# Performance work log

Hardware: AMD Instinct MI355X
Metric: run time of the kernel (lower is better)

## Reference

```python
import jax, jax.numpy as jnp
import numpy as np

# init_kwargs: conv_k=1, scale=1
CONV_K = 1
P = 3 - CONV_K          # scale == 1 branch
PAD_X = (P + 1) // 2    # 1 (applied before: top/left)
PAD_Y = P // 2          # 1 (applied after: bottom/right)


def setup_inputs() -> dict:
    key = jax.random.key(0)
    x = jax.random.normal(key, (16, 256, 128, 128), dtype=jnp.float32)
    return {"x": x}


def reference(x):
    # Fixed FIR kernel f = [1,3,3,1]; norm_fir_k -> 2D outer product, normalized.
    f1 = jnp.array([1.0, 3.0, 3.0, 1.0], dtype=x.dtype)
    k = jnp.outer(f1, f1)
    k = k / jnp.sum(k)
    # upfirdn2d performs true convolution (kernel flipped); symmetric here but kept for fidelity.
    k = jnp.flip(k, (0, 1))
    C = x.shape[1]
    w = jnp.broadcast_to(k[None, None], (C, 1, 4, 4))  # depthwise filter
    out = jax.lax.conv_general_dilated(
        x, w,
        window_strides=(1, 1),
        padding=((PAD_X, PAD_Y), (PAD_X, PAD_Y)),
        feature_group_count=C,
        dimension_numbers=("NCHW", "OIHW", "NCHW"),
    )
    # out: [16, 256, 127, 127] = H + padX + padY - 4 + 1
    return out
```

## Files before the change

### kernel.cpp

```cpp
#include <hip/hip_runtime.h>


#define IH 128
#define IW 128
#define OH 127
#define OW 127

__global__ __launch_bounds__(128)
void upfirdn2d_blur_kernel(const float* __restrict__ x, float* __restrict__ out) {
    const int img = blockIdx.x;
    const int tx  = threadIdx.x;

    const float* __restrict__ in = x   + (size_t)img * (IH * IW);
    float*       __restrict__ o  = out + (size_t)img * (OH * OW);

    const bool active = (tx < OW);

    const float mL = (tx >= 1)      ? 1.0f : 0.0f;
    const float mR = (tx + 2 < IW)  ? 1.0f : 0.0f;
    const int xl = (tx >= 1)      ? tx - 1 : 0;
    const int x1 = (tx + 1 < IW)  ? tx + 1 : IW - 1;
    const int xr = (tx + 2 < IW)  ? tx + 2 : IW - 1;

    auto hrow = [&](int r) -> float {
        const float* __restrict__ p = in + r * IW;
        return mL * p[xl] + 3.0f * (p[tx] + p[x1]) + mR * p[xr];
    };

    float hm1 = 0.0f;
    float h0  = hrow(0);
    float h1  = hrow(1);

    #pragma unroll 2
    for (int y = 0; y < OH - 1; ++y) {
        const float h2 = hrow(y + 2);
        if (active)
            o[y * OW + tx] = (hm1 + 3.0f * (h0 + h1) + h2) * 0.015625f;
        hm1 = h0; h0 = h1; h1 = h2;
    }
    if (active)
        o[(OH - 1) * OW + tx] = (hm1 + 3.0f * (h0 + h1)) * 0.015625f;
}

extern "C" void kernel_launch(void* const* d_in, const int* in_sizes, int n_in,
                              void* d_out, int out_size, void* d_ws, size_t ws_size,
                              hipStream_t stream) {
    const float* x = (const float*)d_in[0];
    float* out = (float*)d_out;
    const int n_imgs = 16 * 256;
    hipLaunchKernelGGL(upfirdn2d_blur_kernel, dim3(n_imgs), dim3(128), 0, stream,
                       x, out);
}
```

Baseline: 473.7 us.

## Vectorize blur with float4 row loads, wave shuffles, and row-split threads

Each thread now loads four adjacent input pixels as a float4 and gets its horizontal neighbours through wave shuffles, so the redundant overlapping scalar loads go away. Each image's 128 threads are split into four groups of 32 lanes, and each group handles a 32-row band with its own halo rows. This cuts load instruction count and gives more independent streams per block. The cost is recomputing two halo rows per band, and the output stores stay scalar and unaligned because the output row width is 127.

```diff
diff --git a/kernel.cpp b/kernel.cpp
--- a/kernel.cpp
+++ b/kernel.cpp
@@ -1,53 +1,77 @@
 #include <hip/hip_runtime.h>
 
 
+#define IW 128
 #define IH 128
-#define IW 128
+#define OW 127
 #define OH 127
-#define OW 127
 
 __global__ __launch_bounds__(128)
-void upfirdn2d_blur_kernel(const float* __restrict__ x, float* __restrict__ out) {
+void upfirdn2d_blur_v2(const float4* __restrict__ x, float* __restrict__ out) {
+    const int tid = threadIdx.x;
+    const int c   = tid & 31;
+    const int s   = tid >> 5;
     const int img = blockIdx.x;
-    const int tx  = threadIdx.x;
 
-    const float* __restrict__ in = x   + (size_t)img * (IH * IW);
-    float*       __restrict__ o  = out + (size_t)img * (OH * OW);
+    const float4* __restrict__ in4 = x + (size_t)img * (IH * IW / 4);
+    float*        __restrict__ o   = out + (size_t)img * (OH * OW);
 
-    const bool active = (tx < OW);
+    const float mL = (c > 0)  ? 1.0f : 0.0f;
+    const float mR = (c < 31) ? 1.0f : 0.0f;
+    const int lm1 = (tid - 1) & 63;
+    const int lp1 = (tid + 1) & 63;
 
-    const float mL = (tx >= 1)      ? 1.0f : 0.0f;
-    const float mR = (tx + 2 < IW)  ? 1.0f : 0.0f;
-    const int xl = (tx >= 1)      ? tx - 1 : 0;
-    const int x1 = (tx + 1 < IW)  ? tx + 1 : IW - 1;
-    const int xr = (tx + 2 < IW)  ? tx + 2 : IW - 1;
-
-    auto hrow = [&](int r) -> float {
-        const float* __restrict__ p = in + r * IW;
-        return mL * p[xl] + 3.0f * (p[tx] + p[x1]) + mR * p[xr];
+    auto hrow = [&](int r) -> float4 {
+        const float4 v = in4[r * (IW / 4) + c];
+        const float l  = mL * __shfl(v.w, lm1, 64);
+        const float r0 = mR * __shfl(v.x, lp1, 64);
+        const float r1 = mR * __shfl(v.y, lp1, 64);
+        float4 h;
+        h.x = l   + 3.0f * (v.x + v.y) + v.z;
+        h.y = v.x + 3.0f * (v.y + v.z) + v.w;
+        h.z = v.y + 3.0f * (v.z + v.w) + r0;
+        h.w = v.z + 3.0f * (v.w + r0)  + r1;
+        return h;
     };
 
-    float hm1 = 0.0f;
-    float h0  = hrow(0);
-    float h1  = hrow(1);
+    const int y0 = 32 * s;
 
-    #pragma unroll 2
-    for (int y = 0; y < OH - 1; ++y) {
-        const float h2 = hrow(y + 2);
-        if (active)
-            o[y * OW + tx] = (hm1 + 3.0f * (h0 + h1) + h2) * 0.015625f;
+    float4 hm1 = hrow(y0 > 0 ? y0 - 1 : 0);
+    const float mTop = (y0 > 0) ? 1.0f : 0.0f;
+    hm1.x *= mTop; hm1.y *= mTop; hm1.z *= mTop; hm1.w *= mTop;
+    float4 h0 = hrow(y0);
+    float4 h1 = hrow(y0 + 1);
+
+    #pragma unroll 4
+    for (int i = 0; i < 32; ++i) {
+        const int y  = y0 + i;
+        const int r2 = y + 2;
+        const float m2 = (r2 < IH) ? 1.0f : 0.0f;
+        float4 h2 = hrow(r2 < IH ? r2 : IH - 1);
+        h2.x *= m2; h2.y *= m2; h2.z *= m2; h2.w *= m2;
+
+        if (y < OH) {
+            float4 r;
+            r.x = (hm1.x + 3.0f * (h0.x + h1.x) + h2.x) * 0.015625f;
+            r.y = (hm1.y + 3.0f * (h0.y + h1.y) + h2.y) * 0.015625f;
+            r.z = (hm1.z + 3.0f * (h0.z + h1.z) + h2.z) * 0.015625f;
+            r.w = (hm1.w + 3.0f * (h0.w + h1.w) + h2.w) * 0.015625f;
+            float* __restrict__ po = o + y * OW + 4 * c;
+            po[0] = r.x;
+            po[1] = r.y;
+            po[2] = r.z;
+            if (c < 31) po[3] = r.w;
+        }
         hm1 = h0; h0 = h1; h1 = h2;
     }
-    if (active)
-        o[(OH - 1) * OW + tx] = (hm1 + 3.0f * (h0 + h1)) * 0.015625f;
 }
 
 extern "C" void kernel_launch(void* const* d_in, const int* in_sizes, int n_in,
                               void* d_out, int out_size, void* d_ws, size_t ws_size,
                               hipStream_t stream) {
-    const float* x = (const float*)d_in[0];
+    const float4* x = (const float4*)d_in[0];
     float* out = (float*)d_out;
     const int n_imgs = 16 * 256;
-    hipLaunchKernelGGL(upfirdn2d_blur_kernel, dim3(n_imgs), dim3(128), 0, stream,
+    hipLaunchKernelGGL(upfirdn2d_blur_v2, dim3(n_imgs), dim3(128), 0, stream,
                        x, out);
 }
```

New measurement: 459.6 us. 1.03x faster.
